# Kernel tuning notes

Measured on AMD Instinct MI355X. Metric: run time of the kernel, lower is better.

## Reference

```python
import jax, jax.numpy as jnp
import numpy as np

C = 256
C8 = C // 8


def setup_inputs() -> dict:
    key = jax.random.key(0)
    ks = jax.random.split(key, 8)
    B, H, W = 4, 64, 64
    s = 0.05
    return {
        "x": jax.random.normal(ks[0], (B, C, H, W), jnp.float32),
        "Wq": jax.random.normal(ks[1], (C8, C), jnp.float32) * s,
        "bq": jax.random.normal(ks[2], (C8,), jnp.float32) * s,
        "Wk": jax.random.normal(ks[3], (C8, C), jnp.float32) * s,
        "bk": jax.random.normal(ks[4], (C8,), jnp.float32) * s,
        "Wv": jax.random.normal(ks[5], (C, C), jnp.float32) * s,
        "bv": jax.random.normal(ks[6], (C,), jnp.float32) * s,
        "gamma": jnp.zeros((1,), jnp.float32),
    }


def reference(x, Wq, bq, Wk, bk, Wv, bv, gamma):
    B, Ch, H, W = x.shape
    N = H * W
    xf = x.reshape(B, Ch, N)  # [B,C,N]
    # 1x1 convs == channel-mixing matmuls
    q = jnp.einsum("oc,bcn->bon", Wq, xf) + bq[None, :, None]  # [B,C8,N]
    k = jnp.einsum("oc,bcn->bon", Wk, xf) + bk[None, :, None]  # [B,C8,N]
    v = jnp.einsum("oc,bcn->bon", Wv, xf) + bv[None, :, None]  # [B,C,N]
    # energy[b,i,j] = sum_c q[b,c,i] * k[b,c,j]  (unscaled, as in original)
    energy = jnp.einsum("bci,bcj->bij", q, k)  # [B,N,N]
    attention = jax.nn.softmax(energy, axis=-1)  # softmax over j
    # out[b,c,i] = sum_j v[b,c,j] * attention[b,i,j]
    out = jnp.einsum("bcj,bij->bci", v, attention).reshape(B, Ch, H, W)
    out = gamma[0] * out + x
    attention_map = attention[0]
    return out, attention_map
```

## Files before the change

kernel.cpp:

```cpp
#include <hip/hip_runtime.h>
#include <hip/hip_bf16.h>
#include <cstdint>
#include <cstddef>

#define C_    256
#define C8_   32
#define NPIX  4096
#define BATCH 4
#define OUT_ELEMS (BATCH * C_ * NPIX)

typedef short bf16x8 __attribute__((ext_vector_type(8)));
typedef float f32x4  __attribute__((ext_vector_type(4)));
typedef unsigned uint32x2 __attribute__((ext_vector_type(2)));

#define LOG2E 1.44269504088896340736f

#define PROW 520

static __device__ __forceinline__ unsigned short f2bf(float f) {
    union { float f; unsigned u; } v; v.f = f;
    unsigned r = v.u + 0x7fff + ((v.u >> 16) & 1);
    return (unsigned short)(r >> 16);
}

static __device__ __forceinline__ unsigned pack_bf2(float p0, float p1) {
    union { float f; unsigned u; } a, b; a.f = p0; b.f = p1;
    return __builtin_amdgcn_perm(b.u, a.u, 0x07060302u);
}
static __device__ __forceinline__ float unpk_lo(unsigned u) {
    union { unsigned u; float f; } v; v.u = u << 16; return v.f;
}
static __device__ __forceinline__ float unpk_hi(unsigned u) {
    union { unsigned u; float f; } v; v.u = u & 0xffff0000u; return v.f;
}

static __device__ __forceinline__ f32x4 mfma16(bf16x8 a, bf16x8 b, f32x4 c) {
    return __builtin_amdgcn_mfma_f32_16x16x32_bf16(a, b, c, 0, 0, 0);
}

__global__ __launch_bounds__(256) void k_pre(
    const float* __restrict__ x,
    const float* __restrict__ Wq, const float* __restrict__ bq,
    const float* __restrict__ Wk, const float* __restrict__ bk,
    const float* __restrict__ Wv, const float* __restrict__ bv,
    const float* __restrict__ gamma,
    float* __restrict__ out,
    unsigned short* __restrict__ qT,
    unsigned short* __restrict__ kT,
    unsigned short* __restrict__ vB)
{
    __shared__ float xs[256][64];
    __shared__ float pred[4][8][64];

    const int bid = blockIdx.x;
    const float gval = gamma[0];

    if (bid < 2048) {
        const size_t base = (size_t)bid * 256 + threadIdx.x;
        const f32x4* src = (const f32x4*)x;
        f32x4* dst = (f32x4*)out;
        f32x4 a = src[base];
        f32x4 b = src[base + 524288];
        __builtin_nontemporal_store(a, dst + base);
        __builtin_nontemporal_store(b, dst + base + 524288);
        return;
    }

    if (bid < 4096) {
        const int idx = bid - 2048;
        const int b   = idx >> 9;
        if (gval == 0.0f && b > 0) return;
        const int sub  = idx & 511;
        const int og8  = sub >> 6;
        const int n0   = (sub & 63) * 64;
        const bool is_q = (og8 < 4);
        const int obase = (og8 & 3) * 8;

        const int tl = threadIdx.x & 15;
        const int tr = threadIdx.x >> 4;
        const float* xb = x + (size_t)b * C_ * NPIX + n0;
        f32x4 v[16];
#pragma unroll
        for (int p = 0; p < 16; ++p)
            v[p] = *(const f32x4*)(xb + (size_t)(p * 16 + tr) * NPIX + tl * 4);
#pragma unroll
        for (int p = 0; p < 16; ++p)
            *(f32x4*)&xs[p * 16 + tr][tl * 4] = v[p];
        __syncthreads();

        const int wv = __builtin_amdgcn_readfirstlane(threadIdx.x >> 6);
        const int ln = threadIdx.x & 63;
        const float* Wb = (is_q ? Wq : Wk);
        float acc[8] = {0.f, 0.f, 0.f, 0.f, 0.f, 0.f, 0.f, 0.f};
#pragma unroll 8
        for (int cc = 0; cc < 64; ++cc) {
            const int c = wv * 64 + cc;
            const float xv = xs[c][ln];
#pragma unroll
            for (int o = 0; o < 8; ++o)
                acc[o] = fmaf(Wb[(size_t)(obase + o) * C_ + c], xv, acc[o]);
        }
#pragma unroll
        for (int o = 0; o < 8; ++o) pred[wv][o][ln] = acc[o];
        __syncthreads();

        const int o1 = threadIdx.x >> 6;
        const int n  = threadIdx.x & 63;
#pragma unroll
        for (int k = 0; k < 2; ++k) {
            const int ol = o1 + k * 4;
            const int oa = obase + ol;
            float s = pred[0][ol][n] + pred[1][ol][n] +
                      pred[2][ol][n] + pred[3][ol][n];
            if (is_q) {
                s = (s + bq[oa]) * LOG2E;
                qT[((size_t)b * NPIX + n0 + n) * C8_ + oa] = f2bf(s);
            } else {
                s = s + bk[oa];
                kT[((size_t)b * NPIX + n0 + n) * C8_ + oa] = f2bf(s);
            }
        }
        return;
    }

    {
        if (gval == 0.0f) return;
        const int idx = bid - 4096;
        const int b   = idx >> 10;
        const int rem = idx & 1023;
        const int w   = threadIdx.x >> 6;
        const int o0  = ((rem >> 6) * 4 + w) * 4;
        const int n   = (rem & 63) * 64 + (threadIdx.x & 63);

        float acc[4];
#pragma unroll
        for (int m = 0; m < 4; ++m) acc[m] = bv[o0 + m];
        const float* xb = x + (size_t)b * C_ * NPIX + n;
#pragma unroll 4
        for (int c = 0; c < C_; ++c) {
            float xv = xb[(size_t)c * NPIX];
#pragma unroll
            for (int m = 0; m < 4; ++m) acc[m] = fmaf(Wv[(o0 + m) * C_ + c], xv, acc[m]);
        }
#pragma unroll
        for (int m = 0; m < 4; ++m)
            vB[((size_t)b * C_ + o0 + m) * NPIX + n] = f2bf(acc[m]);
    }
}

__global__ __launch_bounds__(512) void k_attn3(
    const float* __restrict__ x,
    const unsigned short* __restrict__ qT,
    const unsigned short* __restrict__ kT,
    const unsigned short* __restrict__ vB,
    const float* __restrict__ gamma,
    float* __restrict__ out,
    float* __restrict__ attn)
{
    const int b = blockIdx.y;
    const float g = gamma[0];
    if (g == 0.0f && b > 0) return;

    const int i0   = blockIdx.x * 16;
    const int t    = threadIdx.x;
    const int lane = t & 63;
    const int wavei = __builtin_amdgcn_readfirstlane(t >> 6);
    const int li   = lane & 15;
    const int lg   = lane >> 4;

    __shared__ unsigned short pbuf[8 * 16 * PROW];
    __shared__ float red[8][16];

    const unsigned short* qTb = qT + (size_t)b * NPIX * C8_;
    const unsigned short* kTb = kT + (size_t)b * NPIX * C8_;

    bf16x8 qf = *(const bf16x8*)(qTb + (size_t)(i0 + li) * C8_ + lg * 8);

    const int jw = wavei * 512;
    unsigned short* prow = pbuf + (size_t)(wavei * 16 + li) * PROW;

    float ssum = 0.f;
#pragma unroll
    for (int s = 0; s < 32; ++s) {
        bf16x8 kf = *(const bf16x8*)(kTb + (size_t)(jw + s * 16 + li) * C8_ + lg * 8);
        f32x4 z = {0.f, 0.f, 0.f, 0.f};
        f32x4 e = mfma16(kf, qf, z);
        float p0 = exp2f(e[0]);
        float p1 = exp2f(e[1]);
        float p2 = exp2f(e[2]);
        float p3 = exp2f(e[3]);
        ssum += (p0 + p1) + (p2 + p3);
        uint32x2 pk;
        pk.x = pack_bf2(p0, p1);
        pk.y = pack_bf2(p2, p3);
        *(uint32x2*)(prow + s * 16 + lg * 4) = pk;
    }

    ssum += __shfl_xor(ssum, 16, 64);
    ssum += __shfl_xor(ssum, 32, 64);
    if (lane < 16) red[wavei][lane] = ssum;
    __syncthreads();
    float l = 0.f;
#pragma unroll
    for (int w = 0; w < 8; ++w) l += red[w][li];
    const float inv = 1.0f / l;

    if (b == 0) {
#pragma unroll
        for (int r = 0; r < 16; ++r) {
            const float inv_r = __shfl(inv, r, 64);
            const unsigned short* rp = pbuf + (size_t)(wavei * 16 + r) * PROW;
            float* ap = attn + (size_t)(i0 + r) * NPIX + jw;
            uint32x2 u0 = *(const uint32x2*)(rp + lane * 4);
            uint32x2 u1 = *(const uint32x2*)(rp + 256 + lane * 4);
            f32x4 v0, v1;
            v0[0] = unpk_lo(u0.x) * inv_r; v0[1] = unpk_hi(u0.x) * inv_r;
            v0[2] = unpk_lo(u0.y) * inv_r; v0[3] = unpk_hi(u0.y) * inv_r;
            v1[0] = unpk_lo(u1.x) * inv_r; v1[1] = unpk_hi(u1.x) * inv_r;
            v1[2] = unpk_lo(u1.y) * inv_r; v1[3] = unpk_hi(u1.y) * inv_r;
            __builtin_nontemporal_store(v0, (f32x4*)(ap + lane * 4));
            __builtin_nontemporal_store(v1, (f32x4*)(ap + 256 + lane * 4));
        }
    }

    if (g != 0.0f) {
        f32x4 o0 = {0.f, 0.f, 0.f, 0.f};
        f32x4 o1 = {0.f, 0.f, 0.f, 0.f};
        const unsigned short* vb = vB + (size_t)b * C_ * NPIX;
        for (int st = 0; st < 8; ++st) {
            const int jbase = st * 512;
#pragma unroll
            for (int ks = 0; ks < 16; ++ks) {
                bf16x8 af = *(const bf16x8*)(pbuf + (size_t)(st * 16 + li) * PROW +
                                             ks * 32 + lg * 8);
                const unsigned short* vp0 =
                    vb + (size_t)(wavei * 32 + li) * NPIX + jbase + ks * 32 + lg * 8;
                bf16x8 vf0 = *(const bf16x8*)vp0;
                o0 = mfma16(af, vf0, o0);
                bf16x8 vf1 = *(const bf16x8*)(vp0 + (size_t)16 * NPIX);
                o1 = mfma16(af, vf1, o1);
            }
        }
        const float* xbt = x + (size_t)b * C_ * NPIX;
        float* outb = out + (size_t)b * C_ * NPIX;
        f32x4 sc;
#pragma unroll
        for (int r = 0; r < 4; ++r) sc[r] = g * __shfl(inv, lg * 4 + r, 64);
        {
            int c = wavei * 32 + li;
            f32x4 xv = *(const f32x4*)(xbt + (size_t)c * NPIX + i0 + lg * 4);
            f32x4 r0 = o0 * sc + xv;
            *(f32x4*)(outb + (size_t)c * NPIX + i0 + lg * 4) = r0;
            c += 16;
            f32x4 xv1 = *(const f32x4*)(xbt + (size_t)c * NPIX + i0 + lg * 4);
            f32x4 r1 = o1 * sc + xv1;
            *(f32x4*)(outb + (size_t)c * NPIX + i0 + lg * 4) = r1;
        }
    }
}

extern "C" void kernel_launch(void* const* d_in, const int* in_sizes, int n_in,
                              void* d_out, int out_size, void* d_ws, size_t ws_size,
                              hipStream_t stream) {
    (void)in_sizes; (void)n_in; (void)out_size; (void)ws_size;
    const float* x     = (const float*)d_in[0];
    const float* Wq    = (const float*)d_in[1];
    const float* bq    = (const float*)d_in[2];
    const float* Wk    = (const float*)d_in[3];
    const float* bk    = (const float*)d_in[4];
    const float* Wv    = (const float*)d_in[5];
    const float* bv    = (const float*)d_in[6];
    const float* gamma = (const float*)d_in[7];

    float* out  = (float*)d_out;
    float* attn = out + OUT_ELEMS;

    unsigned short* qT = (unsigned short*)d_ws;
    unsigned short* kT = qT + (size_t)BATCH * NPIX * C8_;
    unsigned short* vB = kT + (size_t)BATCH * NPIX * C8_;

    k_pre<<<8192, 256, 0, stream>>>(x, Wq, bq, Wk, bk, Wv, bv, gamma,
                                    out, qT, kT, vB);

    dim3 g2(NPIX / 16, BATCH);
    k_attn3<<<g2, 512, 0, stream>>>(x, qT, kT, vB, gamma, out, attn);
}
```

Before: 34.02 us.

## Halve attention LDS buffer with two-phase P staging; move residual copy into idle blocks

The probability buffer is cut to half width, so each wave keeps the second half of its exponentiated scores in registers and writes them into LDS only after the first half has been consumed by the PV product and the attention-map store. The smaller shared-memory footprint, together with the launch-bounds hint of 4 blocks, is meant to let more attention blocks run at once per CU. The x-to-out residual copy moves from the projection kernel into the attention blocks that return early when gamma is zero. This adds extra barriers and register pressure from the 16-entry staging array, and the copy now runs only on that gamma-zero path.

```diff
diff --git a/kernel.cpp b/kernel.cpp
--- a/kernel.cpp
+++ b/kernel.cpp
@@ -15,7 +15,7 @@
 
 #define LOG2E 1.44269504088896340736f
 
-#define PROW 520
+#define PROW 264
 
 static __device__ __forceinline__ unsigned short f2bf(float f) {
     union { float f; unsigned u; } v; v.f = f;
@@ -38,13 +38,12 @@
     return __builtin_amdgcn_mfma_f32_16x16x32_bf16(a, b, c, 0, 0, 0);
 }
 
-__global__ __launch_bounds__(256) void k_pre(
+__global__ __launch_bounds__(256) void k_proj(
     const float* __restrict__ x,
     const float* __restrict__ Wq, const float* __restrict__ bq,
     const float* __restrict__ Wk, const float* __restrict__ bk,
     const float* __restrict__ Wv, const float* __restrict__ bv,
     const float* __restrict__ gamma,
-    float* __restrict__ out,
     unsigned short* __restrict__ qT,
     unsigned short* __restrict__ kT,
     unsigned short* __restrict__ vB)
@@ -56,18 +55,7 @@
     const float gval = gamma[0];
 
     if (bid < 2048) {
-        const size_t base = (size_t)bid * 256 + threadIdx.x;
-        const f32x4* src = (const f32x4*)x;
-        f32x4* dst = (f32x4*)out;
-        f32x4 a = src[base];
-        f32x4 b = src[base + 524288];
-        __builtin_nontemporal_store(a, dst + base);
-        __builtin_nontemporal_store(b, dst + base + 524288);
-        return;
-    }
-
-    if (bid < 4096) {
-        const int idx = bid - 2048;
+        const int idx = bid;
         const int b   = idx >> 9;
         if (gval == 0.0f && b > 0) return;
         const int sub  = idx & 511;
@@ -125,7 +113,7 @@
 
     {
         if (gval == 0.0f) return;
-        const int idx = bid - 4096;
+        const int idx = bid - 2048;
         const int b   = idx >> 10;
         const int rem = idx & 1023;
         const int w   = threadIdx.x >> 6;
@@ -148,7 +136,7 @@
     }
 }
 
-__global__ __launch_bounds__(512) void k_attn3(
+__global__ __launch_bounds__(512, 4) void k_attn4(
     const float* __restrict__ x,
     const unsigned short* __restrict__ qT,
     const unsigned short* __restrict__ kT,
@@ -159,7 +147,20 @@
 {
     const int b = blockIdx.y;
     const float g = gamma[0];
-    if (g == 0.0f && b > 0) return;
+
+    __shared__ unsigned short pbuf[8 * 16 * PROW];
+    __shared__ float red[8][16];
+
+    if (g == 0.0f && b > 0) {
+        const int cb = (b - 1) * 256 + blockIdx.x;
+        const size_t n4 = (size_t)OUT_ELEMS / 4;
+        const f32x4* src = (const f32x4*)x;
+        f32x4* dst = (f32x4*)out;
+        for (size_t i = (size_t)cb * 512 + threadIdx.x; i < n4;
+             i += (size_t)768 * 512)
+            __builtin_nontemporal_store(src[i], dst + i);
+        return;
+    }
 
     const int i0   = blockIdx.x * 16;
     const int t    = threadIdx.x;
@@ -168,9 +169,6 @@
     const int li   = lane & 15;
     const int lg   = lane >> 4;
 
-    __shared__ unsigned short pbuf[8 * 16 * PROW];
-    __shared__ float red[8][16];
-
     const unsigned short* qTb = qT + (size_t)b * NPIX * C8_;
     const unsigned short* kTb = kT + (size_t)b * NPIX * C8_;
 
@@ -181,20 +179,30 @@
 
     float ssum = 0.f;
 #pragma unroll
-    for (int s = 0; s < 32; ++s) {
+    for (int s = 0; s < 16; ++s) {
         bf16x8 kf = *(const bf16x8*)(kTb + (size_t)(jw + s * 16 + li) * C8_ + lg * 8);
         f32x4 z = {0.f, 0.f, 0.f, 0.f};
         f32x4 e = mfma16(kf, qf, z);
-        float p0 = exp2f(e[0]);
-        float p1 = exp2f(e[1]);
-        float p2 = exp2f(e[2]);
-        float p3 = exp2f(e[3]);
+        float p0 = exp2f(e[0]), p1 = exp2f(e[1]);
+        float p2 = exp2f(e[2]), p3 = exp2f(e[3]);
         ssum += (p0 + p1) + (p2 + p3);
         uint32x2 pk;
         pk.x = pack_bf2(p0, p1);
         pk.y = pack_bf2(p2, p3);
         *(uint32x2*)(prow + s * 16 + lg * 4) = pk;
     }
+    uint32x2 sp2[16];
+#pragma unroll
+    for (int s = 0; s < 16; ++s) {
+        bf16x8 kf = *(const bf16x8*)(kTb + (size_t)(jw + 256 + s * 16 + li) * C8_ + lg * 8);
+        f32x4 z = {0.f, 0.f, 0.f, 0.f};
+        f32x4 e = mfma16(kf, qf, z);
+        float p0 = exp2f(e[0]), p1 = exp2f(e[1]);
+        float p2 = exp2f(e[2]), p3 = exp2f(e[3]);
+        ssum += (p0 + p1) + (p2 + p3);
+        sp2[s].x = pack_bf2(p0, p1);
+        sp2[s].y = pack_bf2(p2, p3);
+    }
 
     ssum += __shfl_xor(ssum, 16, 64);
     ssum += __shfl_xor(ssum, 32, 64);
@@ -205,40 +213,72 @@
     for (int w = 0; w < 8; ++w) l += red[w][li];
     const float inv = 1.0f / l;
 
+    const bool do_pv = (g != 0.0f);
+    f32x4 o0 = {0.f, 0.f, 0.f, 0.f};
+    f32x4 o1 = {0.f, 0.f, 0.f, 0.f};
+    const unsigned short* vb = vB + (size_t)b * C_ * NPIX;
+
     if (b == 0) {
 #pragma unroll
         for (int r = 0; r < 16; ++r) {
             const float inv_r = __shfl(inv, r, 64);
             const unsigned short* rp = pbuf + (size_t)(wavei * 16 + r) * PROW;
-            float* ap = attn + (size_t)(i0 + r) * NPIX + jw;
-            uint32x2 u0 = *(const uint32x2*)(rp + lane * 4);
-            uint32x2 u1 = *(const uint32x2*)(rp + 256 + lane * 4);
-            f32x4 v0, v1;
-            v0[0] = unpk_lo(u0.x) * inv_r; v0[1] = unpk_hi(u0.x) * inv_r;
-            v0[2] = unpk_lo(u0.y) * inv_r; v0[3] = unpk_hi(u0.y) * inv_r;
-            v1[0] = unpk_lo(u1.x) * inv_r; v1[1] = unpk_hi(u1.x) * inv_r;
-            v1[2] = unpk_lo(u1.y) * inv_r; v1[3] = unpk_hi(u1.y) * inv_r;
-            __builtin_nontemporal_store(v0, (f32x4*)(ap + lane * 4));
-            __builtin_nontemporal_store(v1, (f32x4*)(ap + 256 + lane * 4));
-        }
-    }
-
-    if (g != 0.0f) {
-        f32x4 o0 = {0.f, 0.f, 0.f, 0.f};
-        f32x4 o1 = {0.f, 0.f, 0.f, 0.f};
-        const unsigned short* vb = vB + (size_t)b * C_ * NPIX;
+            uint32x2 u = *(const uint32x2*)(rp + lane * 4);
+            f32x4 v4;
+            v4[0] = unpk_lo(u.x) * inv_r; v4[1] = unpk_hi(u.x) * inv_r;
+            v4[2] = unpk_lo(u.y) * inv_r; v4[3] = unpk_hi(u.y) * inv_r;
+            __builtin_nontemporal_store(
+                v4, (f32x4*)(attn + (size_t)(i0 + r) * NPIX + jw + lane * 4));
+        }
+    }
+    if (do_pv) {
+#pragma unroll
         for (int st = 0; st < 8; ++st) {
-            const int jbase = st * 512;
-#pragma unroll
-            for (int ks = 0; ks < 16; ++ks) {
+#pragma unroll
+            for (int ks = 0; ks < 8; ++ks) {
                 bf16x8 af = *(const bf16x8*)(pbuf + (size_t)(st * 16 + li) * PROW +
                                              ks * 32 + lg * 8);
-                const unsigned short* vp0 =
-                    vb + (size_t)(wavei * 32 + li) * NPIX + jbase + ks * 32 + lg * 8;
-                bf16x8 vf0 = *(const bf16x8*)vp0;
-                o0 = mfma16(af, vf0, o0);
-                bf16x8 vf1 = *(const bf16x8*)(vp0 + (size_t)16 * NPIX);
-                o1 = mfma16(af, vf1, o1);
+                const int j = st * 512 + ks * 32 + lg * 8;
+                const unsigned short* vp0 = vb + (size_t)(wavei * 32 + li) * NPIX + j;
+                o0 = mfma16(af, *(const bf16x8*)vp0, o0);
+                o1 = mfma16(af, *(const bf16x8*)(vp0 + (size_t)16 * NPIX), o1);
+            }
+        }
+        __syncthreads();
+    } else {
+        asm volatile("s_waitcnt lgkmcnt(0)" ::: "memory");
+    }
+
+#pragma unroll
+    for (int s = 0; s < 16; ++s)
+        *(uint32x2*)(prow + s * 16 + lg * 4) = sp2[s];
+    if (do_pv) __syncthreads();
+
+    if (b == 0) {
+        if (!do_pv) { asm volatile("s_waitcnt lgkmcnt(0)" ::: "memory"); }
+#pragma unroll
+        for (int r = 0; r < 16; ++r) {
+            const float inv_r = __shfl(inv, r, 64);
+            const unsigned short* rp = pbuf + (size_t)(wavei * 16 + r) * PROW;
+            uint32x2 u = *(const uint32x2*)(rp + lane * 4);
+            f32x4 v4;
+            v4[0] = unpk_lo(u.x) * inv_r; v4[1] = unpk_hi(u.x) * inv_r;
+            v4[2] = unpk_lo(u.y) * inv_r; v4[3] = unpk_hi(u.y) * inv_r;
+            __builtin_nontemporal_store(
+                v4, (f32x4*)(attn + (size_t)(i0 + r) * NPIX + jw + 256 + lane * 4));
+        }
+    }
+    if (do_pv) {
+#pragma unroll
+        for (int st = 0; st < 8; ++st) {
+#pragma unroll
+            for (int ks = 0; ks < 8; ++ks) {
+                bf16x8 af = *(const bf16x8*)(pbuf + (size_t)(st * 16 + li) * PROW +
+                                             ks * 32 + lg * 8);
+                const int j = st * 512 + 256 + ks * 32 + lg * 8;
+                const unsigned short* vp0 = vb + (size_t)(wavei * 32 + li) * NPIX + j;
+                o0 = mfma16(af, *(const bf16x8*)vp0, o0);
+                o1 = mfma16(af, *(const bf16x8*)(vp0 + (size_t)16 * NPIX), o1);
             }
         }
         const float* xbt = x + (size_t)b * C_ * NPIX;
@@ -279,9 +319,9 @@
     unsigned short* kT = qT + (size_t)BATCH * NPIX * C8_;
     unsigned short* vB = kT + (size_t)BATCH * NPIX * C8_;
 
-    k_pre<<<8192, 256, 0, stream>>>(x, Wq, bq, Wk, bk, Wv, bv, gamma,
-                                    out, qT, kT, vB);
+    k_proj<<<6144, 256, 0, stream>>>(x, Wq, bq, Wk, bk, Wv, bv, gamma,
+                                     qT, kT, vB);
 
     dim3 g2(NPIX / 16, BATCH);
-    k_attn3<<<g2, 512, 0, stream>>>(x, qT, kT, vB, gamma, out, attn);
-}
+    k_attn4<<<g2, 512, 0, stream>>>(x, qT, kT, vB, gamma, out, attn);
+}
```

New measurement: 32.61 us. 4.1% less time.
